# Kernel optimization log

Hardware: AMD Instinct MI355X
Metric: run time of the kernel (lower is better)

Reference implementation:

```python
import jax, jax.numpy as jnp
import numpy as np

B, C, T = 32, 1536, 2048
BN = 128  # bottleneck channels


def setup_inputs() -> dict:
    key = jax.random.key(0)
    k1, k2, k3, k4, k5, k6 = jax.random.split(key, 6)
    x = jax.random.normal(k1, (B, C, T), dtype=jnp.float32)
    padding_mask = jax.random.randint(k2, (B, T), 0, 2) == 1
    W_tdnn = jax.random.normal(k3, (BN, C), dtype=jnp.float32) * (1.0 / np.sqrt(C))
    b_tdnn = jax.random.normal(k4, (BN,), dtype=jnp.float32) * 0.01
    W_attn = jax.random.normal(k5, (C, BN), dtype=jnp.float32) * (1.0 / np.sqrt(BN))
    b_attn = jax.random.normal(k6, (C,), dtype=jnp.float32) * 0.01
    return {"x": x, "padding_mask": padding_mask, "W_tdnn": W_tdnn,
            "b_tdnn": b_tdnn, "W_attn": W_attn, "b_attn": b_attn}


def reference(x, padding_mask, W_tdnn, b_tdnn, W_attn, b_attn):
    # pointwise conv1 (k=1) == channel-wise matmul: (B,C,T) -> (B,BN,T)
    e = jnp.tanh(jnp.einsum('oc,bct->bot', W_tdnn, x) + b_tdnn[None, :, None])
    # pointwise conv2: (B,BN,T) -> (B,C,T)
    a = jnp.einsum('co,bot->bct', W_attn, e) + b_attn[None, :, None]
    a = jnp.where(padding_mask[:, None, :], -1e9, a)
    alpha = jax.nn.softmax(a, axis=2)  # (B,C,T)
    mean = jnp.sum(alpha * x, axis=2)  # (B,C)
    var = jnp.sum(alpha * (x - mean[:, :, None]) ** 2, axis=2)
    std = jnp.sqrt(jnp.clip(var, 1e-9, None))
    return jnp.concatenate([mean, std], axis=1)  # (B,2C)
```

## Files before the change

### kernel.cpp

```cpp
#include <hip/hip_runtime.h>
#include <math.h>

#define Bn  32
#define Cn  1536
#define Tn  2048
#define BNn 128
#define SHIFT 12.0f

typedef __attribute__((ext_vector_type(8))) short bf16x8;
typedef __attribute__((ext_vector_type(4))) float fx4;

__device__ __forceinline__ unsigned int f2bf1(float f) {
    unsigned int u = __float_as_uint(f);
    return (u + 0x7fffu + ((u >> 16) & 1u)) >> 16;
}
__device__ __forceinline__ float fast_tanh(float v) {
    return 1.f - 2.f / (__expf(2.f * v) + 1.f);
}

__global__ void k_prep(const float* __restrict__ W1f, const float* __restrict__ Waf,
                       short* __restrict__ W1b, short* __restrict__ Wab,
                       float* __restrict__ accp) {
    int i = blockIdx.x * 256 + threadIdx.x;
    if (i < BNn * Cn) {
        W1b[i] = (short)f2bf1(W1f[i]);
        Wab[i] = (short)f2bf1(Waf[i]);
    }
    if (i < Bn * Cn)
        *(float4*)&accp[(size_t)i * 4] = make_float4(0.f, 0.f, 0.f, 0.f);
}

__device__ __forceinline__ void stage_w1(short* sW, const short* __restrict__ W1,
                                         int tid, int k0) {
    #pragma unroll
    for (int j = 0; j < 4; ++j) {
        const int o   = (tid >> 3) + j * 32;
        const int blk = (tid & 7) ^ (o & 7);
        __builtin_amdgcn_global_load_lds(
            (const __attribute__((address_space(1))) unsigned int*)
                (W1 + (size_t)o * Cn + k0 + blk * 8),
            (__attribute__((address_space(3))) unsigned int*)(sW + tid * 8 + j * 2048),
            16, 0, 0);
    }
}


#define P1_LOAD(XR, K0) do {                                                  \
    _Pragma("unroll") for (int p = 0; p < 2; ++p) {                           \
        const int c_ = cq + p * 32;                                           \
        _Pragma("unroll") for (int j = 0; j < 4; ++j)                         \
            XR[p][j] = *(const float4*)(xt + (size_t)((K0) + c_ + j) * Tn + t4); \
    }                                                                         \
} while (0)

#define P1_WRITE(XR) do {                                                     \
    _Pragma("unroll") for (int p = 0; p < 2; ++p) {                           \
        const int c_   = cq + p * 32;                                         \
        const int blk_ = c_ >> 3;                                             \
        const int sub_ = c_ & 7;                                              \
        _Pragma("unroll") for (int i2 = 0; i2 < 4; ++i2) {                    \
            const int t_ = t4 + i2;                                           \
            unsigned int lo_ = f2bf1(((const float*)&XR[p][0])[i2]) |         \
                               (f2bf1(((const float*)&XR[p][1])[i2]) << 16);  \
            unsigned int hi_ = f2bf1(((const float*)&XR[p][2])[i2]) |         \
                               (f2bf1(((const float*)&XR[p][3])[i2]) << 16);  \
            const int idx_ = t_ * 64 + ((blk_ ^ (t_ & 7)) << 3) + sub_;       \
            *(uint2*)(sA + idx_) = make_uint2(lo_, hi_);                      \
        }                                                                     \
    }                                                                         \
} while (0)

#define P1_COMPUTE(SW) do {                                                   \
    _Pragma("unroll") for (int kt = 0; kt < 2; ++kt) {                        \
        bf16x8 bq_[4];                                                        \
        _Pragma("unroll") for (int nn = 0; nn < 4; ++nn) {                    \
            const int o_ = wo + nn * 16 + ln;                                 \
            bq_[nn] = *(const bf16x8*)((SW) + o_ * 64                         \
                                       + (((kt * 4 + g) ^ (o_ & 7)) << 3));   \
        }                                                                     \
        bf16x8 af_[4];                                                        \
        _Pragma("unroll") for (int mm = 0; mm < 4; ++mm) {                    \
            const int t_ = wt + mm * 16 + ln;                                 \
            af_[mm] = *(const bf16x8*)(sA + t_ * 64                           \
                                       + (((kt * 4 + g) ^ (t_ & 7)) << 3));   \
        }                                                                     \
        _Pragma("unroll") for (int mm = 0; mm < 4; ++mm)                      \
            _Pragma("unroll") for (int nn = 0; nn < 4; ++nn)                  \
                acc[mm][nn] = __builtin_amdgcn_mfma_f32_16x16x32_bf16(        \
                    af_[mm], bq_[nn], acc[mm][nn], 0, 0, 0);                  \
    }                                                                         \
} while (0)

#define P2_CR(I) (((Cn - 64) - ((I) >> 1) * 64) + wc + ((I) & 1) * 16 + ln)

#define P2_LOAD(BQ, XQ, I) do {                                               \
    const int cr_ = P2_CR(I);                                                 \
    _Pragma("unroll") for (int kt = 0; kt < 4; ++kt)                          \
        BQ[kt] = *(const bf16x8*)(Wab + (size_t)cr_ * BNn + kt * 32 + g * 8); \
    _Pragma("unroll") for (int mt = 0; mt < 4; ++mt)                          \
        XQ[mt] = *(const float4*)(xb + (size_t)cr_ * Tn                       \
                                  + t0g + wt + mt * 16 + g * 4);              \
} while (0)

#define P2_COMPUTE(BQ, XQ, I) do {                                           \
    fx4 a2_[4];                                                               \
    _Pragma("unroll") for (int mt = 0; mt < 4; ++mt)                          \
        a2_[mt] = (fx4){0.f, 0.f, 0.f, 0.f};                                  \
    _Pragma("unroll") for (int kt = 0; kt < 4; ++kt)                          \
        _Pragma("unroll") for (int mt = 0; mt < 4; ++mt)                      \
            a2_[mt] = __builtin_amdgcn_mfma_f32_16x16x32_bf16(                \
                af2[mt][kt], BQ[kt], a2_[mt], 0, 0, 0);                       \
    float s0_ = 0.f, s1_ = 0.f, s2_ = 0.f;                                    \
    _Pragma("unroll") for (int mt = 0; mt < 4; ++mt) {                        \
        _Pragma("unroll") for (int r = 0; r < 4; ++r) {                       \
            const int msk_ = ((const int*)&mv[mt])[r];                        \
            const float p_ = msk_ ? 0.f : __expf(a2_[mt][r] - SHIFT);         \
            const float xv_ = ((const float*)&XQ[mt])[r];                     \
            s0_ += p_; s1_ += p_ * xv_; s2_ += p_ * xv_ * xv_;                \
        }                                                                     \
    }                                                                         \
    s0_ += __shfl_xor(s0_, 16); s1_ += __shfl_xor(s1_, 16);                   \
    s2_ += __shfl_xor(s2_, 16);                                               \
    s0_ += __shfl_xor(s0_, 32); s1_ += __shfl_xor(s1_, 32);                   \
    s2_ += __shfl_xor(s2_, 32);                                               \
    if (g == 0) {                                                             \
        float* ap_ = accp + ((size_t)b * Cn + P2_CR(I)) * 4;                  \
        atomicAdd(ap_ + 0, s0_);                                              \
        atomicAdd(ap_ + 1, s1_);                                              \
        atomicAdd(ap_ + 2, s2_);                                              \
    }                                                                         \
} while (0)

__global__ __launch_bounds__(256, 2) void k_fused(
    const float* __restrict__ x, const short* __restrict__ W1,
    const float* __restrict__ bias, const short* __restrict__ Wab,
    const int* __restrict__ mask, float* __restrict__ accp)
{
    __shared__ short sA[128 * 64];
    __shared__ short sE[128 * 128];

    const int b    = blockIdx.y;
    const int t0g  = blockIdx.x * 128;
    const int tid  = threadIdx.x;
    const int lane = tid & 63;
    const int wv   = tid >> 6;
    const int ln   = lane & 15;
    const int g    = lane >> 4;
    const int wt   = (wv & 1) * 64;
    const int wo   = (wv >> 1) * 64;

    const float* xb = x + (size_t)b * Cn * Tn;
    const float* xt = xb + t0g;

    const int t4 = (tid & 31) * 4;
    const int cq = (tid >> 5) * 4;

    short* const sW0 = sE;
    short* const sW1 = sE + 8192;

    fx4 acc[4][4];
    #pragma unroll
    for (int i = 0; i < 4; ++i)
        #pragma unroll
        for (int j = 0; j < 4; ++j) acc[i][j] = (fx4){0.f, 0.f, 0.f, 0.f};

    float4 xr[2][4];
    stage_w1(sW0, W1, tid, 0);
    P1_LOAD(xr, 0);

    for (int i = 0; i < Cn / 64; ++i) {
        const int k0 = i * 64;
        short* const sWc = (i & 1) ? sW1 : sW0;
        short* const sWn = (i & 1) ? sW0 : sW1;
        __syncthreads();
        P1_WRITE(xr);
        __syncthreads();
        if (i + 1 < Cn / 64) {
            stage_w1(sWn, W1, tid, k0 + 64);
            P1_LOAD(xr, k0 + 64);
        }
        P1_COMPUTE(sWc);
    }
    __syncthreads();

    float bs[4];
    #pragma unroll
    for (int nn = 0; nn < 4; ++nn) bs[nn] = bias[wo + nn * 16 + ln];

    #pragma unroll
    for (int mm = 0; mm < 4; ++mm)
        #pragma unroll
        for (int nn = 0; nn < 4; ++nn) {
            #pragma unroll
            for (int r = 0; r < 4; ++r) {
                const int t = wt + mm * 16 + g * 4 + r;
                const int o = wo + nn * 16 + ln;
                const float v = fast_tanh(acc[mm][nn][r] + bs[nn]);
                sE[t * 128 + (((o >> 3) ^ (t & 15)) << 3) + (o & 7)] = (short)f2bf1(v);
            }
        }
    __syncthreads();

    bf16x8 af2[4][4];
    #pragma unroll
    for (int mt = 0; mt < 4; ++mt)
        #pragma unroll
        for (int kt = 0; kt < 4; ++kt) {
            const int t = wt + mt * 16 + ln;
            af2[mt][kt] = *(const bf16x8*)(sE + t * 128 + (((kt * 4 + g) ^ (t & 15)) << 3));
        }

    int4 mv[4];
    #pragma unroll
    for (int mt = 0; mt < 4; ++mt)
        mv[mt] = *(const int4*)(mask + (size_t)b * Tn + t0g + wt + mt * 16 + g * 4);

    const int wc = (wv >> 1) * 32;

    bf16x8 bA[4], bB[4];
    float4 xA[4], xB[4];
    P2_LOAD(bA, xA, 0);
    for (int i = 0; i < 48; i += 2) {
        P2_LOAD(bB, xB, i + 1);
        P2_COMPUTE(bA, xA, i);
        if (i + 2 < 48) P2_LOAD(bA, xA, i + 2);
        P2_COMPUTE(bB, xB, i + 1);
    }
}

__global__ void k_final(const float* __restrict__ accp, float* __restrict__ out) {
    const int i = blockIdx.x * 256 + threadIdx.x;
    if (i >= Bn * Cn) return;
    const int b = i / Cn, c = i - b * Cn;
    const float4 v = *(const float4*)&accp[(size_t)i * 4];
    const float mean = v.y / v.x;
    const float var  = fmaxf(v.z / v.x - mean * mean, 1e-9f);
    out[(size_t)b * (2 * Cn) + c]      = mean;
    out[(size_t)b * (2 * Cn) + Cn + c] = sqrtf(var);
}

extern "C" void kernel_launch(void* const* d_in, const int* in_sizes, int n_in,
                              void* d_out, int out_size, void* d_ws, size_t ws_size,
                              hipStream_t stream) {
    const float* x      = (const float*)d_in[0];
    const int*   mask   = (const int*)d_in[1];
    const float* W_tdnn = (const float*)d_in[2];
    const float* b_tdnn = (const float*)d_in[3];
    const float* W_attn = (const float*)d_in[4];
    float* out = (float*)d_out;

    short* W1b  = (short*)d_ws;
    short* Wab  = W1b + (size_t)BNn * Cn;
    float* accp = (float*)(Wab + (size_t)BNn * Cn);

    k_prep<<<dim3((BNn * Cn + 255) / 256), 256, 0, stream>>>(W_tdnn, W_attn, W1b, Wab, accp);
    k_fused<<<dim3(Tn / 128, Bn), 256, 0, stream>>>(x, W1b, b_tdnn, Wab, mask, accp);
    k_final<<<dim3((Bn * Cn + 255) / 256), 256, 0, stream>>>(accp, out);
}
```

Baseline: 633.5 us.

## Halve fused kernel T-tile to 64 and raise occupancy to four blocks per CU

Cuts the time tile per block from 128 to 64, which halves the per-thread accumulator, fragment and prefetch register arrays and shrinks shared memory. Launch bounds go from two to four blocks per CU to hide memory latency. The W tile buffers are reused for the tanh output, and the swizzle on the x tile is changed to fit the new 64-row layout. The cost is twice as many blocks, each restaging the full W1 and reloading Wab. Phase 1 does half the MFMA work per W-tile load, and there are twice as many atomics into the accumulator.

```diff
diff --git a/kernel.cpp b/kernel.cpp
--- a/kernel.cpp
+++ b/kernel.cpp
@@ -17,6 +17,8 @@
 __device__ __forceinline__ float fast_tanh(float v) {
     return 1.f - 2.f / (__expf(2.f * v) + 1.f);
 }
+
+#define SWZA(T) (((T) ^ ((T) >> 2)) & 7)
 
 __global__ void k_prep(const float* __restrict__ W1f, const float* __restrict__ Waf,
                        short* __restrict__ W1b, short* __restrict__ Wab,
@@ -45,28 +47,22 @@
 }
 
 
-#define P1_LOAD(XR, K0) do {                                                  \
-    _Pragma("unroll") for (int p = 0; p < 2; ++p) {                           \
-        const int c_ = cq + p * 32;                                           \
-        _Pragma("unroll") for (int j = 0; j < 4; ++j)                         \
-            XR[p][j] = *(const float4*)(xt + (size_t)((K0) + c_ + j) * Tn + t4); \
-    }                                                                         \
-} while (0)
-
-#define P1_WRITE(XR) do {                                                     \
-    _Pragma("unroll") for (int p = 0; p < 2; ++p) {                           \
-        const int c_   = cq + p * 32;                                         \
-        const int blk_ = c_ >> 3;                                             \
-        const int sub_ = c_ & 7;                                              \
-        _Pragma("unroll") for (int i2 = 0; i2 < 4; ++i2) {                    \
-            const int t_ = t4 + i2;                                           \
-            unsigned int lo_ = f2bf1(((const float*)&XR[p][0])[i2]) |         \
-                               (f2bf1(((const float*)&XR[p][1])[i2]) << 16);  \
-            unsigned int hi_ = f2bf1(((const float*)&XR[p][2])[i2]) |         \
-                               (f2bf1(((const float*)&XR[p][3])[i2]) << 16);  \
-            const int idx_ = t_ * 64 + ((blk_ ^ (t_ & 7)) << 3) + sub_;       \
-            *(uint2*)(sA + idx_) = make_uint2(lo_, hi_);                      \
-        }                                                                     \
+#define P1_LOAD(K0) do {                                                      \
+    _Pragma("unroll") for (int j = 0; j < 4; ++j)                             \
+        xr[j] = *(const float4*)(xt + (size_t)((K0) + cq + j) * Tn + t4);     \
+} while (0)
+
+#define P1_WRITE() do {                                                       \
+    const int blk_ = cq >> 3;                                                 \
+    const int sub_ = cq & 7;                                                  \
+    _Pragma("unroll") for (int i2 = 0; i2 < 4; ++i2) {                        \
+        const int t_ = t4 + i2;                                               \
+        unsigned int lo_ = f2bf1(((const float*)&xr[0])[i2]) |                \
+                           (f2bf1(((const float*)&xr[1])[i2]) << 16);         \
+        unsigned int hi_ = f2bf1(((const float*)&xr[2])[i2]) |                \
+                           (f2bf1(((const float*)&xr[3])[i2]) << 16);         \
+        const int idx_ = t_ * 64 + ((blk_ ^ SWZA(t_)) << 3) + sub_;           \
+        *(uint2*)(sA + idx_) = make_uint2(lo_, hi_);                          \
     }                                                                         \
 } while (0)
 
@@ -78,13 +74,13 @@
             bq_[nn] = *(const bf16x8*)((SW) + o_ * 64                         \
                                        + (((kt * 4 + g) ^ (o_ & 7)) << 3));   \
         }                                                                     \
-        bf16x8 af_[4];                                                        \
-        _Pragma("unroll") for (int mm = 0; mm < 4; ++mm) {                    \
+        bf16x8 af_[2];                                                        \
+        _Pragma("unroll") for (int mm = 0; mm < 2; ++mm) {                    \
             const int t_ = wt + mm * 16 + ln;                                 \
             af_[mm] = *(const bf16x8*)(sA + t_ * 64                           \
-                                       + (((kt * 4 + g) ^ (t_ & 7)) << 3));   \
+                                       + (((kt * 4 + g) ^ SWZA(t_)) << 3));   \
         }                                                                     \
-        _Pragma("unroll") for (int mm = 0; mm < 4; ++mm)                      \
+        _Pragma("unroll") for (int mm = 0; mm < 2; ++mm)                      \
             _Pragma("unroll") for (int nn = 0; nn < 4; ++nn)                  \
                 acc[mm][nn] = __builtin_amdgcn_mfma_f32_16x16x32_bf16(        \
                     af_[mm], bq_[nn], acc[mm][nn], 0, 0, 0);                  \
@@ -97,21 +93,21 @@
     const int cr_ = P2_CR(I);                                                 \
     _Pragma("unroll") for (int kt = 0; kt < 4; ++kt)                          \
         BQ[kt] = *(const bf16x8*)(Wab + (size_t)cr_ * BNn + kt * 32 + g * 8); \
-    _Pragma("unroll") for (int mt = 0; mt < 4; ++mt)                          \
+    _Pragma("unroll") for (int mt = 0; mt < 2; ++mt)                          \
         XQ[mt] = *(const float4*)(xb + (size_t)cr_ * Tn                       \
                                   + t0g + wt + mt * 16 + g * 4);              \
 } while (0)
 
 #define P2_COMPUTE(BQ, XQ, I) do {                                           \
-    fx4 a2_[4];                                                               \
-    _Pragma("unroll") for (int mt = 0; mt < 4; ++mt)                          \
+    fx4 a2_[2];                                                               \
+    _Pragma("unroll") for (int mt = 0; mt < 2; ++mt)                          \
         a2_[mt] = (fx4){0.f, 0.f, 0.f, 0.f};                                  \
     _Pragma("unroll") for (int kt = 0; kt < 4; ++kt)                          \
-        _Pragma("unroll") for (int mt = 0; mt < 4; ++mt)                      \
+        _Pragma("unroll") for (int mt = 0; mt < 2; ++mt)                      \
             a2_[mt] = __builtin_amdgcn_mfma_f32_16x16x32_bf16(                \
                 af2[mt][kt], BQ[kt], a2_[mt], 0, 0, 0);                       \
     float s0_ = 0.f, s1_ = 0.f, s2_ = 0.f;                                    \
-    _Pragma("unroll") for (int mt = 0; mt < 4; ++mt) {                        \
+    _Pragma("unroll") for (int mt = 0; mt < 2; ++mt) {                        \
         _Pragma("unroll") for (int r = 0; r < 4; ++r) {                       \
             const int msk_ = ((const int*)&mv[mt])[r];                        \
             const float p_ = msk_ ? 0.f : __expf(a2_[mt][r] - SHIFT);         \
@@ -131,53 +127,51 @@
     }                                                                         \
 } while (0)
 
-__global__ __launch_bounds__(256, 2) void k_fused(
+__global__ __launch_bounds__(256, 4) void k_fused(
     const float* __restrict__ x, const short* __restrict__ W1,
     const float* __restrict__ bias, const short* __restrict__ Wab,
     const int* __restrict__ mask, float* __restrict__ accp)
 {
-    __shared__ short sA[128 * 64];
-    __shared__ short sE[128 * 128];
+    __shared__ short sA[64 * 64];
+    __shared__ short sW[2][128 * 64];
+    short* const sE = &sW[0][0];
 
     const int b    = blockIdx.y;
-    const int t0g  = blockIdx.x * 128;
+    const int t0g  = blockIdx.x * 64;
     const int tid  = threadIdx.x;
     const int lane = tid & 63;
     const int wv   = tid >> 6;
     const int ln   = lane & 15;
     const int g    = lane >> 4;
-    const int wt   = (wv & 1) * 64;
+    const int wt   = (wv & 1) * 32;
     const int wo   = (wv >> 1) * 64;
 
     const float* xb = x + (size_t)b * Cn * Tn;
     const float* xt = xb + t0g;
 
-    const int t4 = (tid & 31) * 4;
-    const int cq = (tid >> 5) * 4;
-
-    short* const sW0 = sE;
-    short* const sW1 = sE + 8192;
-
-    fx4 acc[4][4];
-    #pragma unroll
-    for (int i = 0; i < 4; ++i)
+    const int t4 = (tid & 15) * 4;
+    const int cq = (tid >> 4) * 4;
+
+    fx4 acc[2][4];
+    #pragma unroll
+    for (int i = 0; i < 2; ++i)
         #pragma unroll
         for (int j = 0; j < 4; ++j) acc[i][j] = (fx4){0.f, 0.f, 0.f, 0.f};
 
-    float4 xr[2][4];
-    stage_w1(sW0, W1, tid, 0);
-    P1_LOAD(xr, 0);
+    float4 xr[4];
+    stage_w1(sW[0], W1, tid, 0);
+    P1_LOAD(0);
 
     for (int i = 0; i < Cn / 64; ++i) {
         const int k0 = i * 64;
-        short* const sWc = (i & 1) ? sW1 : sW0;
-        short* const sWn = (i & 1) ? sW0 : sW1;
+        short* const sWc = sW[i & 1];
+        short* const sWn = sW[(i & 1) ^ 1];
         __syncthreads();
-        P1_WRITE(xr);
+        P1_WRITE();
         __syncthreads();
         if (i + 1 < Cn / 64) {
             stage_w1(sWn, W1, tid, k0 + 64);
-            P1_LOAD(xr, k0 + 64);
+            P1_LOAD(k0 + 64);
         }
         P1_COMPUTE(sWc);
     }
@@ -188,7 +182,7 @@
     for (int nn = 0; nn < 4; ++nn) bs[nn] = bias[wo + nn * 16 + ln];
 
     #pragma unroll
-    for (int mm = 0; mm < 4; ++mm)
+    for (int mm = 0; mm < 2; ++mm)
         #pragma unroll
         for (int nn = 0; nn < 4; ++nn) {
             #pragma unroll
@@ -201,24 +195,24 @@
         }
     __syncthreads();
 
-    bf16x8 af2[4][4];
-    #pragma unroll
-    for (int mt = 0; mt < 4; ++mt)
+    bf16x8 af2[2][4];
+    #pragma unroll
+    for (int mt = 0; mt < 2; ++mt)
         #pragma unroll
         for (int kt = 0; kt < 4; ++kt) {
             const int t = wt + mt * 16 + ln;
             af2[mt][kt] = *(const bf16x8*)(sE + t * 128 + (((kt * 4 + g) ^ (t & 15)) << 3));
         }
 
-    int4 mv[4];
-    #pragma unroll
-    for (int mt = 0; mt < 4; ++mt)
+    int4 mv[2];
+    #pragma unroll
+    for (int mt = 0; mt < 2; ++mt)
         mv[mt] = *(const int4*)(mask + (size_t)b * Tn + t0g + wt + mt * 16 + g * 4);
 
     const int wc = (wv >> 1) * 32;
 
     bf16x8 bA[4], bB[4];
-    float4 xA[4], xB[4];
+    float4 xA[2], xB[2];
     P2_LOAD(bA, xA, 0);
     for (int i = 0; i < 48; i += 2) {
         P2_LOAD(bB, xB, i + 1);
@@ -254,6 +248,6 @@
     float* accp = (float*)(Wab + (size_t)BNn * Cn);
 
     k_prep<<<dim3((BNn * Cn + 255) / 256), 256, 0, stream>>>(W_tdnn, W_attn, W1b, Wab, accp);
-    k_fused<<<dim3(Tn / 128, Bn), 256, 0, stream>>>(x, W1b, b_tdnn, Wab, mask, accp);
+    k_fused<<<dim3(Tn / 64, Bn), 256, 0, stream>>>(x, W1b, b_tdnn, Wab, mask, accp);
     k_final<<<dim3((Bn * Cn + 255) / 256), 256, 0, stream>>>(accp, out);
 }
```

New measurement: 714.9 us. +12.8%, slower.
